# Kernel optimization log

Measured on AMD Instinct MI355X. Metric: run time of the kernel, lower is better.

The kernel has to match this reference:

```python
import jax, jax.numpy as jnp
import numpy as np

B, S, DIM = 2, 2048, 1024
N_HEADS, HEAD_DIM = 16, 64
ROPE_THETA = 10000.0


def _rope_cos_sin(seq_len, head_dim, dtype=jnp.float32):
    inv_freq = 1.0 / (ROPE_THETA ** (jnp.arange(0, head_dim, 2, dtype=jnp.float32) / head_dim))
    ang = jnp.arange(seq_len, dtype=jnp.float32)[:, None] * inv_freq[None, :]  # [S, D/2]
    return jnp.cos(ang).astype(dtype), jnp.sin(ang).astype(dtype)


def _apply_rope(t, cos, sin):
    # t: [B, S, H, D]; cos/sin: [S, D/2]
    t1 = t[..., 0::2]
    t2 = t[..., 1::2]
    c = cos[None, :, None, :]
    s = sin[None, :, None, :]
    r1 = t1 * c - t2 * s
    r2 = t1 * s + t2 * c
    # interleave back to original even/odd layout
    return jnp.stack([r1, r2], axis=-1).reshape(t.shape)


def setup_inputs() -> dict:
    key = jax.random.key(0)
    ks = jax.random.split(key, 5)
    scale = 1.0 / np.sqrt(DIM)
    return {
        "x": jax.random.normal(ks[0], (B, S, DIM), dtype=jnp.float32),
        "Wq": jax.random.normal(ks[1], (DIM, DIM), dtype=jnp.float32) * scale,
        "Wk": jax.random.normal(ks[2], (DIM, DIM), dtype=jnp.float32) * scale,
        "Wv": jax.random.normal(ks[3], (DIM, DIM), dtype=jnp.float32) * scale,
        "Wo": jax.random.normal(ks[4], (DIM, DIM), dtype=jnp.float32) * scale,
    }


def reference(x, Wq, Wk, Wv, Wo):
    b, s, _ = x.shape
    q = (x @ Wq.T).reshape(b, s, N_HEADS, HEAD_DIM)
    k = (x @ Wk.T).reshape(b, s, N_HEADS, HEAD_DIM)
    v = (x @ Wv.T).reshape(b, s, N_HEADS, HEAD_DIM)

    cos, sin = _rope_cos_sin(s, HEAD_DIM, dtype=q.dtype)
    q = _apply_rope(q, cos, sin)
    k = _apply_rope(k, cos, sin)

    # [B, H, S, S] scores with causal mask
    attn = jnp.einsum("bqhd,bkhd->bhqk", q, k) / np.sqrt(HEAD_DIM)
    causal = jnp.tril(jnp.ones((s, s), dtype=bool))
    attn = jnp.where(causal[None, None], attn, jnp.float32(-jnp.inf))
    probs = jax.nn.softmax(attn.astype(jnp.float32), axis=-1).astype(q.dtype)

    out = jnp.einsum("bhqk,bkhd->bqhd", probs, v).reshape(b, s, N_HEADS * HEAD_DIM)
    return out @ Wo.T
```

## Files before the change

kernel.cpp:

```cpp
#include <hip/hip_runtime.h>
#include <hip/hip_bf16.h>

#define S_LEN 2048
#define DIMSZ 1024
#define NH    16
#define HD    64

typedef __attribute__((ext_vector_type(8))) short short8v;
typedef __attribute__((ext_vector_type(4))) short short4v;
typedef __attribute__((ext_vector_type(4))) float f32x4;

typedef const __attribute__((address_space(1))) unsigned GU;
typedef __attribute__((address_space(3))) unsigned LU;

__device__ __forceinline__ void gl16(const ushort* g, ushort* l) {
  __builtin_amdgcn_global_load_lds((GU*)g, (LU*)l, 16, 0, 0);
}

__device__ __forceinline__ ushort f2bf(float f) {
  union { float f; unsigned u; } v; v.f = f;
  unsigned u = v.u;
  return (ushort)((u + 0x7FFFu + ((u >> 16) & 1u)) >> 16);
}

__device__ __forceinline__ uint cvtpk(float lo, float hi) {
  uint d;
  asm("v_cvt_pk_bf16_f32 %0, %1, %2" : "=v"(d) : "v"(lo), "v"(hi));
  return d;
}

__global__ __launch_bounds__(256) void cvt_k(
    const float* __restrict__ x, const float* __restrict__ wq,
    const float* __restrict__ wk, const float* __restrict__ wv,
    const float* __restrict__ wo,
    ushort* __restrict__ xb, ushort* __restrict__ wqkvb, ushort* __restrict__ wob)
{
  size_t gid = (size_t)blockIdx.x * 256 + threadIdx.x;
  size_t e0 = gid * 8;
  const float* src; ushort* dst;
  if (e0 < (4u << 20)) { src = x + e0; dst = xb + e0; }
  else if (e0 < (7u << 20)) {
    size_t o = e0 - (4u << 20);
    const float* w = (o < (1u << 20)) ? wq : ((o < (2u << 20)) ? wk : wv);
    src = w + (o & ((1u << 20) - 1)); dst = wqkvb + o;
  } else {
    size_t o = e0 - (7u << 20);
    src = wo + o; dst = wob + o;
  }
  float4 a = *(const float4*)src;
  float4 b = *(const float4*)(src + 4);
  short8v h;
  h[0] = (short)f2bf(a.x); h[1] = (short)f2bf(a.y);
  h[2] = (short)f2bf(a.z); h[3] = (short)f2bf(a.w);
  h[4] = (short)f2bf(b.x); h[5] = (short)f2bf(b.y);
  h[6] = (short)f2bf(b.z); h[7] = (short)f2bf(b.w);
  *(short8v*)dst = h;
}

__global__ __launch_bounds__(256) void rope_table_k(float2* __restrict__ tab) {
  int i = blockIdx.x * 256 + threadIdx.x;
  int f = i >> 11, s = i & (S_LEN - 1);
  float inv = powf(10000.f, -(float)f * (1.f / 32.f));
  float ang = (float)s * inv;
  tab[i] = make_float2(cosf(ang), sinf(ang));
}

#define QSTAGE(c, kt_) do {                                                     \
    int k0_ = (kt_) * 64;                                                       \
    _Pragma("unroll")                                                           \
    for (int j_ = 0; j_ < 4; ++j_) {                                            \
      int R_ = w * 32 + j_ * 8;                                                 \
      gl16(xb + (size_t)(bm + R_ + r8) * DIMSZ + k0_ + cswz, &lA[c][R_ * 64]);  \
      gl16(W  + (size_t)(bn + R_ + r8) * DIMSZ + k0_ + cswz, &lB[c][R_ * 64]);  \
    }                                                                           \
  } while (0)

__global__ __launch_bounds__(256) void gemm_qkv_k(
    const ushort* __restrict__ xb, const ushort* __restrict__ wqkvb,
    ushort* __restrict__ qb, ushort* __restrict__ kb, ushort* __restrict__ vtb,
    const float2* __restrict__ rtab)
{
  __shared__ ushort lA[2][128 * 64];
  __shared__ ushort lB[2][128 * 64];
  const int t = threadIdx.x;
  int id = blockIdx.x;
  int nid = (id & 7) * 96 + (id >> 3);
  const int which = nid >> 8;
  const int bm = ((nid >> 3) & 31) * 128, bn = (nid & 7) * 128;
  const ushort* W = wqkvb + ((size_t)which << 20);
  const int w = t >> 6, l = t & 63, lr = l & 15, lg = l >> 4;
  const int wm = (w >> 1) * 64, wn = (w & 1) * 64;
  const int r8 = l >> 3;
  const int cswz = ((l & 7) ^ r8) * 8;

  f32x4 acc[4][4] = {};

  QSTAGE(0, 0);
  for (int kt = 0; kt < DIMSZ / 64; ++kt) {
    const int cur = kt & 1;
    if (kt + 1 < DIMSZ / 64) {
      QSTAGE(cur ^ 1, kt + 1);
      asm volatile("s_waitcnt vmcnt(8)" ::: "memory");
    } else {
      asm volatile("s_waitcnt vmcnt(0)" ::: "memory");
    }
    __builtin_amdgcn_s_barrier();
    asm volatile("" ::: "memory");
    #pragma unroll
    for (int kk = 0; kk < 2; ++kk) {
      short8v a[4], b[4];
      #pragma unroll
      for (int mt = 0; mt < 4; ++mt) {
        int row = wm + mt * 16 + lr;
        a[mt] = *(const short8v*)((const char*)lA[cur] + row * 128 + ((kk * 64 + lg * 16) ^ ((row & 7) << 4)));
      }
      #pragma unroll
      for (int nt = 0; nt < 4; ++nt) {
        int row = wn + nt * 16 + lr;
        b[nt] = *(const short8v*)((const char*)lB[cur] + row * 128 + ((kk * 64 + lg * 16) ^ ((row & 7) << 4)));
      }
      #pragma unroll
      for (int mt = 0; mt < 4; ++mt)
        #pragma unroll
        for (int nt = 0; nt < 4; ++nt)
          acc[mt][nt] = __builtin_amdgcn_mfma_f32_16x16x32_bf16(b[nt], a[mt], acc[mt][nt], 0, 0, 0);
    }
    __builtin_amdgcn_s_barrier();
    asm volatile("" ::: "memory");
  }

  const int bb = bm >> 11, s_base = bm & (S_LEN - 1);

  if (which == 2) {
    ushort* tb = &lA[0][0];
    #pragma unroll
    for (int mt = 0; mt < 4; ++mt)
      #pragma unroll
      for (int nt = 0; nt < 4; ++nt)
        #pragma unroll
        for (int r = 0; r < 4; ++r) {
          int row = wn + nt * 16 + lg * 4 + r;
          int col = wm + mt * 16 + lr;
          int byte = row * 256 + ((col * 2) ^ (((row >> 2) & 3) << 5));
          *(ushort*)((char*)tb + byte) = f2bf(acc[mt][nt][r]);
        }
    __syncthreads();
    int row = t >> 1, half = t & 1;
    int h = (bn + row) >> 6, d = (bn + row) & 63;
    int swz = ((row >> 2) & 3) << 5;
    ushort* vdst = vtb + ((size_t)(bb * NH + h) * HD + d) * S_LEN + s_base + half * 64;
    #pragma unroll
    for (int j = 0; j < 8; ++j) {
      int kk = j >> 2, lgi = j & 3;
      int b0 = row * 256 + ((half * 128 + kk * 64 + lgi * 8) ^ swz);
      int b1 = row * 256 + ((half * 128 + kk * 64 + 32 + lgi * 8) ^ swz);
      uint2 lo = *(const uint2*)((const char*)tb + b0);
      uint2 hi = *(const uint2*)((const char*)tb + b1);
      uint4 st; st.x = lo.x; st.y = lo.y; st.z = hi.x; st.w = hi.y;
      *(uint4*)(vdst + j * 8) = st;
    }
  } else {
    ushort* dst = (which == 0) ? qb : kb;
    const float QS = (which == 0) ? (0.125f * 1.4426950408889634f) : 1.0f;
    #pragma unroll
    for (int mt = 0; mt < 4; ++mt) {
      int s = s_base + wm + mt * 16 + lr;
      #pragma unroll
      for (int nt = 0; nt < 4; ++nt) {
        int nw = bn + wn + nt * 16 + lg * 4;
        int h = nw >> 6, d0 = nw & 63;
        uint pk[2];
        #pragma unroll
        for (int rp = 0; rp < 2; ++rp) {
          float2 cs = rtab[(d0 >> 1) * S_LEN + rp * S_LEN + s];
          float t1 = acc[mt][nt][2 * rp], t2 = acc[mt][nt][2 * rp + 1];
          float o0 = (t1 * cs.x - t2 * cs.y) * QS;
          float o1 = (t1 * cs.y + t2 * cs.x) * QS;
          pk[rp] = (uint)f2bf(o0) | ((uint)f2bf(o1) << 16);
        }
        uint2 pv; pv.x = pk[0]; pv.y = pk[1];
        *(uint2*)(dst + ((size_t)(bb * NH + h) * S_LEN + s) * HD + d0) = pv;
      }
    }
  }
}

template<bool DIAG>
__device__ __forceinline__ void attn_tile(
    const ushort* lK, const ushort* lV,
    const short8v* qf, f32x4* o, float& m2, float& lsum,
    int lr, int lg, int wrow)
{
  f32x4 sacc[4] = {};
  __builtin_amdgcn_s_setprio(1);
  #pragma unroll
  for (int kk = 0; kk < 2; ++kk)
    #pragma unroll
    for (int jt = 0; jt < 4; ++jt) {
      int row = jt * 16 + lr;
      short8v kf = *(const short8v*)((const char*)lK + row * 128 + ((kk * 64 + lg * 16) ^ ((row & 7) << 4)));
      sacc[jt] = __builtin_amdgcn_mfma_f32_16x16x32_bf16(kf, qf[kk], sacc[jt], 0, 0, 0);
    }
  __builtin_amdgcn_s_setprio(0);

  float v2[4][4];
  #pragma unroll
  for (int jt = 0; jt < 4; ++jt)
    #pragma unroll
    for (int r = 0; r < 4; ++r) {
      float sv = sacc[jt][r];
      if (DIAG && (jt * 16 + lg * 4 + r > wrow + lr)) sv = -3e38f;
      v2[jt][r] = sv;
    }
  float mj[4];
  #pragma unroll
  for (int jt = 0; jt < 4; ++jt)
    mj[jt] = fmaxf(fmaxf(v2[jt][0], v2[jt][1]), fmaxf(v2[jt][2], v2[jt][3]));
  float pmax = fmaxf(fmaxf(mj[0], mj[1]), fmaxf(mj[2], mj[3]));

  const bool need = __any(pmax > m2 + 8.f);
  float mn = m2;
  float so = 1.f;
  if (need) {
    float rmax = pmax;
    rmax = fmaxf(rmax, __shfl_xor(rmax, 16));
    rmax = fmaxf(rmax, __shfl_xor(rmax, 32));
    mn = fmaxf(m2, rmax);
    so = exp2f(m2 - mn);
    m2 = mn;
  }
  float pe[4][4];
  float ps = 0.f;
  #pragma unroll
  for (int jt = 0; jt < 4; ++jt)
    #pragma unroll
    for (int r = 0; r < 4; ++r) {
      pe[jt][r] = exp2f(v2[jt][r] - mn);
      ps += pe[jt][r];
    }
  if (need) {
    lsum = lsum * so + ps;
    #pragma unroll
    for (int r = 0; r < 4; ++r) {
      float sor = __shfl(so, lg * 4 + r);
      #pragma unroll
      for (int dt = 0; dt < 4; ++dt) o[dt][r] *= sor;
    }
  } else {
    lsum += ps;
  }

  __builtin_amdgcn_s_setprio(1);
  #pragma unroll
  for (int kk = 0; kk < 2; ++kk) {
    union { short8v v; uint u[4]; } pu;
    pu.u[0] = cvtpk(pe[2 * kk][0], pe[2 * kk][1]);
    pu.u[1] = cvtpk(pe[2 * kk][2], pe[2 * kk][3]);
    pu.u[2] = cvtpk(pe[2 * kk + 1][0], pe[2 * kk + 1][1]);
    pu.u[3] = cvtpk(pe[2 * kk + 1][2], pe[2 * kk + 1][3]);
    #pragma unroll
    for (int dt = 0; dt < 4; ++dt) {
      int row = dt * 16 + lr;
      short8v vb = *(const short8v*)((const char*)lV + row * 128 + ((kk * 64 + lg * 16) ^ ((row & 7) << 4)));
      o[dt] = __builtin_amdgcn_mfma_f32_16x16x32_bf16(pu.v, vb, o[dt], 0, 0, 0);
    }
  }
  __builtin_amdgcn_s_setprio(0);
}

__device__ __forceinline__ void store_tile(
    ushort* __restrict__ ab, int bh, int qt, int w, int lr, int lg,
    const f32x4* o, float lsum)
{
  float lf = lsum;
  lf += __shfl_xor(lf, 16);
  lf += __shfl_xor(lf, 32);
  int b = bh >> 4, h = bh & 15;
  #pragma unroll
  for (int r = 0; r < 4; ++r) {
    float li = __shfl(lf, lg * 4 + r);
    float inv = 1.f / li;
    int qg = qt * 64 + w * 16 + lg * 4 + r;
    #pragma unroll
    for (int dt = 0; dt < 4; ++dt)
      ab[((size_t)b * S_LEN + qg) * DIMSZ + h * HD + dt * 16 + lr] = f2bf(o[dt][r] * inv);
  }
}

#define STAGE(c, ktile) do {                                                  \
    int kk0_ = (ktile) * 64;                                                  \
    _Pragma("unroll")                                                         \
    for (int j_ = 0; j_ < 2; ++j_) {                                          \
      int R_ = w * 16 + j_ * 8;                                               \
      gl16(kbh + (size_t)(kk0_ + R_ + r8) * HD + cswz, &lKb[c][R_ * 64]);     \
      gl16(vbh + (size_t)(R_ + r8) * S_LEN + kk0_ + cswz, &lVb[c][R_ * 64]);  \
    }                                                                         \
  } while (0)

__global__ __launch_bounds__(256, 4) void flash_k(
    const ushort* __restrict__ qb, const ushort* __restrict__ kb,
    const ushort* __restrict__ vtb, ushort* __restrict__ ab)
{
  __shared__ ushort lKb[2][64 * 64];
  __shared__ ushort lVb[2][64 * 64];

  int id = blockIdx.x;
  int nid = (id & 7) * 128 + (id >> 3);
  const int bh = (nid >> 7) * 4 + (nid & 3);
  const int qt = 31 - ((nid & 127) >> 2);
  const int NT = qt + 1;

  const int t = threadIdx.x, w = t >> 6, l = t & 63, lr = l & 15, lg = l >> 4;
  const int r8 = l >> 3;
  const int cswz = ((l & 7) ^ r8) * 8;
  const ushort* kbh = kb + (size_t)bh * S_LEN * HD;
  const ushort* vbh = vtb + (size_t)bh * HD * S_LEN;

  short8v qf[2];
  #pragma unroll
  for (int kk = 0; kk < 2; ++kk)
    qf[kk] = *(const short8v*)(qb + ((size_t)bh * S_LEN + qt * 64 + w * 16 + lr) * HD + kk * 32 + lg * 8);

  float m2 = -3e38f, lsum = 0.f;
  f32x4 o[4] = {};

  STAGE(0, 0);
  asm volatile("s_waitcnt vmcnt(0)" ::: "memory");
  __builtin_amdgcn_s_barrier();
  asm volatile("" ::: "memory");

  for (int kt = 0; kt < NT; ++kt) {
    const int cur = kt & 1;
    if (kt + 1 < NT) STAGE(cur ^ 1, kt + 1);
    const ushort* lK = lKb[cur];
    const ushort* lV = lVb[cur];
    if (kt == qt) attn_tile<true >(lK, lV, qf, o, m2, lsum, lr, lg, w * 16);
    else          attn_tile<false>(lK, lV, qf, o, m2, lsum, lr, lg, w * 16);
    asm volatile("s_waitcnt vmcnt(0)" ::: "memory");
    __builtin_amdgcn_s_barrier();
    asm volatile("" ::: "memory");
  }

  store_tile(ab, bh, qt, w, lr, lg, o, lsum);
}

#define OSTAGE(c, kt_) do {                                                     \
    int k0_ = (kt_) * 64;                                                       \
    _Pragma("unroll")                                                           \
    for (int j_ = 0; j_ < 4; ++j_) {                                            \
      int R_ = w * 32 + j_ * 8;                                                 \
      gl16(ab  + (size_t)(bm + R_ + r8) * DIMSZ + k0_ + cswz, &lA[c][R_ * 64]); \
      gl16(wob + (size_t)(bn + R_ + r8) * DIMSZ + k0_ + cswz, &lB[c][R_ * 64]); \
    }                                                                           \
  } while (0)

__global__ __launch_bounds__(256) void gemm_out_k(
    const ushort* __restrict__ ab, const ushort* __restrict__ wob, float* __restrict__ out)
{
  __shared__ ushort lA[2][128 * 64];
  __shared__ ushort lB[2][128 * 64];
  const int t = threadIdx.x;
  int id = blockIdx.x;
  int nid = (id & 7) * 32 + (id >> 3);
  const int bm = (nid >> 3) * 128, bn = (nid & 7) * 128;
  const int w = t >> 6, l = t & 63, lr = l & 15, lg = l >> 4;
  const int wm = (w >> 1) * 64, wn = (w & 1) * 64;
  const int r8 = l >> 3;
  const int cswz = ((l & 7) ^ r8) * 8;

  f32x4 acc[4][4] = {};

  OSTAGE(0, 0);
  for (int kt = 0; kt < DIMSZ / 64; ++kt) {
    const int cur = kt & 1;
    if (kt + 1 < DIMSZ / 64) {
      OSTAGE(cur ^ 1, kt + 1);
      asm volatile("s_waitcnt vmcnt(8)" ::: "memory");
    } else {
      asm volatile("s_waitcnt vmcnt(0)" ::: "memory");
    }
    __builtin_amdgcn_s_barrier();
    asm volatile("" ::: "memory");
    #pragma unroll
    for (int kk = 0; kk < 2; ++kk) {
      short8v a[4], b[4];
      #pragma unroll
      for (int mt = 0; mt < 4; ++mt) {
        int row = wm + mt * 16 + lr;
        a[mt] = *(const short8v*)((const char*)lA[cur] + row * 128 + ((kk * 64 + lg * 16) ^ ((row & 7) << 4)));
      }
      #pragma unroll
      for (int nt = 0; nt < 4; ++nt) {
        int row = wn + nt * 16 + lr;
        b[nt] = *(const short8v*)((const char*)lB[cur] + row * 128 + ((kk * 64 + lg * 16) ^ ((row & 7) << 4)));
      }
      #pragma unroll
      for (int mt = 0; mt < 4; ++mt)
        #pragma unroll
        for (int nt = 0; nt < 4; ++nt)
          acc[mt][nt] = __builtin_amdgcn_mfma_f32_16x16x32_bf16(b[nt], a[mt], acc[mt][nt], 0, 0, 0);
    }
    __builtin_amdgcn_s_barrier();
    asm volatile("" ::: "memory");
  }

  #pragma unroll
  for (int mt = 0; mt < 4; ++mt) {
    int m = bm + wm + mt * 16 + lr;
    #pragma unroll
    for (int nt = 0; nt < 4; ++nt) {
      int nb = bn + wn + nt * 16 + lg * 4;
      *(f32x4*)(out + (size_t)m * DIMSZ + nb) = acc[mt][nt];
    }
  }
}

extern "C" void kernel_launch(void* const* d_in, const int* in_sizes, int n_in,
                              void* d_out, int out_size, void* d_ws, size_t ws_size,
                              hipStream_t stream) {
  (void)in_sizes; (void)n_in; (void)out_size; (void)ws_size;
  const float* x  = (const float*)d_in[0];
  const float* Wq = (const float*)d_in[1];
  const float* Wk = (const float*)d_in[2];
  const float* Wv = (const float*)d_in[3];
  const float* Wo = (const float*)d_in[4];
  float* out = (float*)d_out;

  char* ws = (char*)d_ws;
  ushort* qb    = (ushort*)(ws);
  ushort* kb    = (ushort*)(ws + ((size_t)8  << 20));
  ushort* vtb   = (ushort*)(ws + ((size_t)16 << 20));
  ushort* xb    = (ushort*)(ws + ((size_t)24 << 20));
  ushort* ab    = xb;
  ushort* wqkvb = (ushort*)(ws + ((size_t)32 << 20));
  ushort* wob   = (ushort*)(ws + ((size_t)38 << 20));
  float2* rtab  = (float2*)(ws + ((size_t)40 << 20));

  hipLaunchKernelGGL(cvt_k, dim3(4096), dim3(256), 0, stream,
                     x, Wq, Wk, Wv, Wo, xb, wqkvb, wob);
  hipLaunchKernelGGL(rope_table_k, dim3(S_LEN * 32 / 256), dim3(256), 0, stream, rtab);
  hipLaunchKernelGGL(gemm_qkv_k, dim3(768), dim3(256), 0, stream,
                     xb, wqkvb, qb, kb, vtb, rtab);
  hipLaunchKernelGGL(flash_k, dim3(1024), dim3(256), 0, stream, qb, kb, vtb, ab);
  hipLaunchKernelGGL(gemm_out_k, dim3(256), dim3(256), 0, stream, ab, wob, out);
}
```

Measured before the change: 120.4 us.

## Triple-buffer QKV GEMM with K=32 stages and halve output GEMM M tile

The QKV projection GEMM moves from a double-buffered K=64 stage to a three-stage ring of K=32 tiles with a new LDS layout, swizzle and lane offsets. This cuts shared memory per block and raises the occupancy hint to 4 blocks per CU. The output projection GEMM uses 64-row M tiles instead of 128, doubling the grid to 512 blocks so the 256-CU device is better filled. The cost is more barriers per K step, lower arithmetic intensity per tile, and a more intricate staging index calculation.

```diff
diff --git a/kernel.cpp b/kernel.cpp
--- a/kernel.cpp
+++ b/kernel.cpp
@@ -65,74 +65,76 @@
   tab[i] = make_float2(cosf(ang), sinf(ang));
 }
 
-#define QSTAGE(c, kt_) do {                                                     \
-    int k0_ = (kt_) * 64;                                                       \
-    _Pragma("unroll")                                                           \
-    for (int j_ = 0; j_ < 4; ++j_) {                                            \
-      int R_ = w * 32 + j_ * 8;                                                 \
-      gl16(xb + (size_t)(bm + R_ + r8) * DIMSZ + k0_ + cswz, &lA[c][R_ * 64]);  \
-      gl16(W  + (size_t)(bn + R_ + r8) * DIMSZ + k0_ + cswz, &lB[c][R_ * 64]);  \
-    }                                                                           \
+#define QSTAGE(c_, kt_) do {                                                    \
+    int k0_ = (kt_) * 32 + colo;                                                \
+    gl16(xb + (size_t)(bm + rj0     ) * DIMSZ + k0_, shm + (c_)*4096 + w*1024);       \
+    gl16(xb + (size_t)(bm + rj0 + 16) * DIMSZ + k0_, shm + (c_)*4096 + w*1024 + 512); \
+    gl16(Wp + (size_t)(bn + rj0     ) * DIMSZ + k0_, shm + 12288 + (c_)*4096 + w*1024);       \
+    gl16(Wp + (size_t)(bn + rj0 + 16) * DIMSZ + k0_, shm + 12288 + (c_)*4096 + w*1024 + 512); \
   } while (0)
 
-__global__ __launch_bounds__(256) void gemm_qkv_k(
+__global__ __launch_bounds__(256, 4) void gemm_qkv_k(
     const ushort* __restrict__ xb, const ushort* __restrict__ wqkvb,
     ushort* __restrict__ qb, ushort* __restrict__ kb, ushort* __restrict__ vtb,
     const float2* __restrict__ rtab)
 {
-  __shared__ ushort lA[2][128 * 64];
-  __shared__ ushort lB[2][128 * 64];
+  __shared__ ushort shm[6 * 4096];
   const int t = threadIdx.x;
   int id = blockIdx.x;
   int nid = (id & 7) * 96 + (id >> 3);
   const int which = nid >> 8;
   const int bm = ((nid >> 3) & 31) * 128, bn = (nid & 7) * 128;
-  const ushort* W = wqkvb + ((size_t)which << 20);
+  const ushort* Wp = wqkvb + ((size_t)which << 20);
   const int w = t >> 6, l = t & 63, lr = l & 15, lg = l >> 4;
   const int wm = (w >> 1) * 64, wn = (w & 1) * 64;
-  const int r8 = l >> 3;
-  const int cswz = ((l & 7) ^ r8) * 8;
+
+  const int sub  = (l & 7) ^ (l >> 3);
+  const int rj0  = 2 * (w * 16 + (l >> 3)) + (sub >> 2);
+  const int colo = (sub & 3) * 8;
+
+  const int lane_off = (lr >> 1) * 128 + (((((lr & 1) << 2) | lg) ^ (lr >> 1)) << 4);
+  const int wm2 = wm >> 1, wn2 = wn >> 1;
 
   f32x4 acc[4][4] = {};
 
   QSTAGE(0, 0);
-  for (int kt = 0; kt < DIMSZ / 64; ++kt) {
-    const int cur = kt & 1;
-    if (kt + 1 < DIMSZ / 64) {
-      QSTAGE(cur ^ 1, kt + 1);
+  QSTAGE(1, 1);
+  int c0 = 0, c1 = 1, c2 = 2;
+  for (int kt = 0; kt < 32; ++kt) {
+    if (kt + 2 < 32) {
+      QSTAGE(c2, kt + 2);
       asm volatile("s_waitcnt vmcnt(8)" ::: "memory");
+    } else if (kt + 1 < 32) {
+      asm volatile("s_waitcnt vmcnt(4)" ::: "memory");
     } else {
       asm volatile("s_waitcnt vmcnt(0)" ::: "memory");
     }
     __builtin_amdgcn_s_barrier();
     asm volatile("" ::: "memory");
-    #pragma unroll
-    for (int kk = 0; kk < 2; ++kk) {
-      short8v a[4], b[4];
-      #pragma unroll
-      for (int mt = 0; mt < 4; ++mt) {
-        int row = wm + mt * 16 + lr;
-        a[mt] = *(const short8v*)((const char*)lA[cur] + row * 128 + ((kk * 64 + lg * 16) ^ ((row & 7) << 4)));
-      }
-      #pragma unroll
-      for (int nt = 0; nt < 4; ++nt) {
-        int row = wn + nt * 16 + lr;
-        b[nt] = *(const short8v*)((const char*)lB[cur] + row * 128 + ((kk * 64 + lg * 16) ^ ((row & 7) << 4)));
-      }
-      #pragma unroll
-      for (int mt = 0; mt < 4; ++mt)
-        #pragma unroll
-        for (int nt = 0; nt < 4; ++nt)
-          acc[mt][nt] = __builtin_amdgcn_mfma_f32_16x16x32_bf16(b[nt], a[mt], acc[mt][nt], 0, 0, 0);
-    }
+    const char* lAc = (const char*)(shm + c0 * 4096);
+    const char* lBc = (const char*)(shm + 12288 + c0 * 4096);
+    short8v a[4], b[4];
+    #pragma unroll
+    for (int mt = 0; mt < 4; ++mt)
+      a[mt] = *(const short8v*)(lAc + (wm2 + mt * 8) * 128 + lane_off);
+    #pragma unroll
+    for (int nt = 0; nt < 4; ++nt)
+      b[nt] = *(const short8v*)(lBc + (wn2 + nt * 8) * 128 + lane_off);
+    #pragma unroll
+    for (int mt = 0; mt < 4; ++mt)
+      #pragma unroll
+      for (int nt = 0; nt < 4; ++nt)
+        acc[mt][nt] = __builtin_amdgcn_mfma_f32_16x16x32_bf16(b[nt], a[mt], acc[mt][nt], 0, 0, 0);
     __builtin_amdgcn_s_barrier();
     asm volatile("" ::: "memory");
+    int tmp = c0; c0 = c1; c1 = c2; c2 = tmp;
   }
 
   const int bb = bm >> 11, s_base = bm & (S_LEN - 1);
 
   if (which == 2) {
-    ushort* tb = &lA[0][0];
+    ushort* tb = shm;
+    __syncthreads();
     #pragma unroll
     for (int mt = 0; mt < 4; ++mt)
       #pragma unroll
@@ -347,35 +349,39 @@
 #define OSTAGE(c, kt_) do {                                                     \
     int k0_ = (kt_) * 64;                                                       \
     _Pragma("unroll")                                                           \
+    for (int j_ = 0; j_ < 2; ++j_) {                                            \
+      int R_ = w * 16 + j_ * 8;                                                 \
+      gl16(ab + (size_t)(bm + R_ + r8) * DIMSZ + k0_ + cswz, &lA[c][R_ * 64]);  \
+    }                                                                           \
+    _Pragma("unroll")                                                           \
     for (int j_ = 0; j_ < 4; ++j_) {                                            \
       int R_ = w * 32 + j_ * 8;                                                 \
-      gl16(ab  + (size_t)(bm + R_ + r8) * DIMSZ + k0_ + cswz, &lA[c][R_ * 64]); \
       gl16(wob + (size_t)(bn + R_ + r8) * DIMSZ + k0_ + cswz, &lB[c][R_ * 64]); \
     }                                                                           \
   } while (0)
 
-__global__ __launch_bounds__(256) void gemm_out_k(
+__global__ __launch_bounds__(256, 4) void gemm_out_k(
     const ushort* __restrict__ ab, const ushort* __restrict__ wob, float* __restrict__ out)
 {
-  __shared__ ushort lA[2][128 * 64];
+  __shared__ ushort lA[2][64 * 64];
   __shared__ ushort lB[2][128 * 64];
   const int t = threadIdx.x;
   int id = blockIdx.x;
-  int nid = (id & 7) * 32 + (id >> 3);
-  const int bm = (nid >> 3) * 128, bn = (nid & 7) * 128;
+  int nid = (id & 7) * 64 + (id >> 3);
+  const int bm = (nid >> 3) * 64, bn = (nid & 7) * 128;
   const int w = t >> 6, l = t & 63, lr = l & 15, lg = l >> 4;
-  const int wm = (w >> 1) * 64, wn = (w & 1) * 64;
+  const int wm = (w >> 1) * 32, wn = (w & 1) * 64;
   const int r8 = l >> 3;
   const int cswz = ((l & 7) ^ r8) * 8;
 
-  f32x4 acc[4][4] = {};
+  f32x4 acc[2][4] = {};
 
   OSTAGE(0, 0);
   for (int kt = 0; kt < DIMSZ / 64; ++kt) {
     const int cur = kt & 1;
     if (kt + 1 < DIMSZ / 64) {
       OSTAGE(cur ^ 1, kt + 1);
-      asm volatile("s_waitcnt vmcnt(8)" ::: "memory");
+      asm volatile("s_waitcnt vmcnt(6)" ::: "memory");
     } else {
       asm volatile("s_waitcnt vmcnt(0)" ::: "memory");
     }
@@ -383,9 +389,9 @@
     asm volatile("" ::: "memory");
     #pragma unroll
     for (int kk = 0; kk < 2; ++kk) {
-      short8v a[4], b[4];
-      #pragma unroll
-      for (int mt = 0; mt < 4; ++mt) {
+      short8v a[2], b[4];
+      #pragma unroll
+      for (int mt = 0; mt < 2; ++mt) {
         int row = wm + mt * 16 + lr;
         a[mt] = *(const short8v*)((const char*)lA[cur] + row * 128 + ((kk * 64 + lg * 16) ^ ((row & 7) << 4)));
       }
@@ -395,7 +401,7 @@
         b[nt] = *(const short8v*)((const char*)lB[cur] + row * 128 + ((kk * 64 + lg * 16) ^ ((row & 7) << 4)));
       }
       #pragma unroll
-      for (int mt = 0; mt < 4; ++mt)
+      for (int mt = 0; mt < 2; ++mt)
         #pragma unroll
         for (int nt = 0; nt < 4; ++nt)
           acc[mt][nt] = __builtin_amdgcn_mfma_f32_16x16x32_bf16(b[nt], a[mt], acc[mt][nt], 0, 0, 0);
@@ -405,7 +411,7 @@
   }
 
   #pragma unroll
-  for (int mt = 0; mt < 4; ++mt) {
+  for (int mt = 0; mt < 2; ++mt) {
     int m = bm + wm + mt * 16 + lr;
     #pragma unroll
     for (int nt = 0; nt < 4; ++nt) {
@@ -442,5 +448,5 @@
   hipLaunchKernelGGL(gemm_qkv_k, dim3(768), dim3(256), 0, stream,
                      xb, wqkvb, qb, kb, vtb, rtab);
   hipLaunchKernelGGL(flash_k, dim3(1024), dim3(256), 0, stream, qb, kb, vtb, ab);
-  hipLaunchKernelGGL(gemm_out_k, dim3(256), dim3(256), 0, stream, ab, wob, out);
-}
+  hipLaunchKernelGGL(gemm_out_k, dim3(512), dim3(256), 0, stream, ab, wob, out);
+}
```

Measured after the change: 116.8 us. -3.0%, faster.
